# Kernel tuning notes

Measured on AMD Instinct MI355X. Metric: run time of the kernel, lower is better.

Reference implementation:

```python
import jax, jax.numpy as jnp
import numpy as np

EMBED = 768
N_HEADS = 12
HEAD = EMBED // N_HEADS  # 64
B, T = 2, 2048


def setup_inputs() -> dict:
    key = jax.random.key(0)
    ks = jax.random.split(key, 5)
    s = 0.02
    return {
        "x": jax.random.normal(ks[0], (B, T, EMBED), dtype=jnp.float32),
        "w_attn": jax.random.normal(ks[1], (EMBED, 3 * EMBED), dtype=jnp.float32) * s,
        "b_attn": jnp.zeros((3 * EMBED,), dtype=jnp.float32),
        "w_proj": jax.random.normal(ks[2], (EMBED, EMBED), dtype=jnp.float32) * s,
        "b_proj": jnp.zeros((EMBED,), dtype=jnp.float32),
    }


def reference(x, w_attn, b_attn, w_proj, b_proj):
    b, t, c = x.shape
    scale = HEAD ** -0.5
    qkv = x @ w_attn + b_attn  # [b,t,3c]
    q, k, v = jnp.split(qkv, 3, axis=-1)

    # einops 'b t (h n) -> b n t h' with n=N_HEADS: channel dim factors as
    # (head_size, n_heads) — head index is the inner factor.
    def split_heads(u):
        return u.reshape(b, t, HEAD, N_HEADS).transpose(0, 3, 1, 2)  # [b,n,t,h]

    q, k, v = split_heads(q), split_heads(k), split_heads(v)

    scores = jnp.einsum("bnth,bnsh->bnts", q, k) * scale  # [b,n,t,t]
    causal = jnp.tril(jnp.ones((t, t), dtype=bool))
    scores = jnp.where(causal, scores, jnp.finfo(scores.dtype).min)
    weights = jax.nn.softmax(scores, axis=-1)
    att = jnp.einsum("bnts,bnsh->bnth", weights, v)  # [b,n,t,h]

    # 'b n t h -> b t (n h)': heads are the OUTER factor on output
    att = att.transpose(0, 2, 1, 3).reshape(b, t, c)
    return att @ w_proj + b_proj
```

## Files before the change

kernel.cpp:

```cpp
#include <hip/hip_runtime.h>
#include <hip/hip_bf16.h>
#include <math.h>

#define NB      2
#define T_SZ    2048
#define EMBEDC  768
#define NHEADS  12
#define HEADD   64
#define QKV_PER (NB * NHEADS * T_SZ * HEADD)
#define QSCALE  0.18033688011112042f

typedef __bf16 bf16x8 __attribute__((ext_vector_type(8)));
typedef float  f32x4  __attribute__((ext_vector_type(4)));
typedef float  f32x16 __attribute__((ext_vector_type(16)));

__device__ inline ushort f2bf(float x) {
    union { float f; uint u; } v; v.f = x;
    uint r = v.u + 0x7fffu + ((v.u >> 16) & 1u);
    return (ushort)(r >> 16);
}

__device__ inline uint pack2bf(float a, float b) {
    union { __bf16 h[2]; uint u; } t;
    t.h[0] = (__bf16)a; t.h[1] = (__bf16)b;
    return t.u;
}

__device__ inline float bflo(uint u) {
    union { uint u; float f; } t; t.u = u << 16; return t.f;
}
__device__ inline float bfhi(uint u) {
    union { uint u; float f; } t; t.u = u & 0xffff0000u; return t.f;
}

__device__ inline void gload16(const ushort* g, ushort* l) {
    __builtin_amdgcn_global_load_lds(
        (const __attribute__((address_space(1))) unsigned int*)g,
        (__attribute__((address_space(3))) unsigned int*)l, 16, 0, 0);
}

__global__ __launch_bounds__(256) void cast_k(const float* __restrict__ in,
                                              ushort* __restrict__ out, int n)
{
    int i = (blockIdx.x * 256 + threadIdx.x) * 8;
    if (i >= n) return;
    float4 a = *(const float4*)(in + i);
    float4 b = *(const float4*)(in + i + 4);
    union { ushort u[8]; int4 v; } p;
    p.u[0] = f2bf(a.x); p.u[1] = f2bf(a.y); p.u[2] = f2bf(a.z); p.u[3] = f2bf(a.w);
    p.u[4] = f2bf(b.x); p.u[5] = f2bf(b.y); p.u[6] = f2bf(b.z); p.u[7] = f2bf(b.w);
    *(int4*)(out + i) = p.v;
}

template <int PERM>
__global__ __launch_bounds__(256) void tcast_k(const float* __restrict__ in,
                                               ushort* __restrict__ out,
                                               int R, int C)
{
    __shared__ float t[32][33];
    const int c0 = blockIdx.x * 32, r0 = blockIdx.y * 32;
    const int tx = threadIdx.x & 31, ty = threadIdx.x >> 5;
#pragma unroll
    for (int u = 0; u < 4; ++u)
        t[ty + 8 * u][tx] = in[(size_t)(r0 + ty + 8 * u) * C + c0 + tx];
    __syncthreads();
#pragma unroll
    for (int u = 0; u < 4; ++u) {
        int n = c0 + ty + 8 * u;
        int orow = n;
        if (PERM) {
            int mat = n / EMBEDC, cc = n % EMBEDC;
            orow = mat * EMBEDC + (cc % NHEADS) * HEADD + cc / NHEADS;
        }
        out[(size_t)orow * R + r0 + tx] = f2bf(t[tx][ty + 8 * u]);
    }
}

__global__ __launch_bounds__(256) void vt_k(const ushort* __restrict__ in,
                                            ushort* __restrict__ out)
{
    __shared__ ushort tile[64][66];
    const int bh = blockIdx.y;
    const int t0 = blockIdx.x * 64;
    const int tid = threadIdx.x;
#pragma unroll
    for (int u = 0; u < 2; ++u) {
        int s = tid + 256 * u;
        int r = s >> 3, c8 = s & 7;
        *(bf16x8*)&tile[r][c8 * 8] =
            *(const bf16x8*)(in + ((size_t)bh * T_SZ + t0 + r) * HEADD + c8 * 8);
    }
    __syncthreads();
#pragma unroll
    for (int u = 0; u < 2; ++u) {
        int s = tid + 256 * u;
        int hd = s >> 3, tt = s & 7;
        union { ushort v[8]; int4 q; } pk;
#pragma unroll
        for (int j = 0; j < 8; ++j) pk.v[j] = tile[tt * 8 + j][hd];
        *(int4*)(out + ((size_t)bh * HEADD + hd) * T_SZ + t0 + tt * 8) = pk.q;
    }
}

#define STAGE(buf, koff)                                        \
    do {                                                        \
        gload16(gA0 + (koff), &As[buf][lA0o]);                  \
        gload16(gA1 + (koff), &As[buf][lA1o]);                  \
        gload16(gB0 + (koff), &Bs[buf][lB0o]);                  \
        gload16(gB1 + (koff), &Bs[buf][lB1o]);                  \
    } while (0)

template <int MODE>
__global__ __launch_bounds__(256) void gemm_bf16_k(
    const ushort* __restrict__ A, const ushort* __restrict__ Bt,
    const float* __restrict__ bias, void* __restrict__ outp,
    int M, int N, int K)
{
    __shared__ ushort As[2][128 * 32];
    __shared__ ushort Bs[2][128 * 32];

    const int tid = threadIdx.x;
    const int w = tid >> 6, l = tid & 63;
    const int g = l >> 4, r16 = l & 15;
    const int wr = w >> 1, wc = w & 1;
    const int m0 = blockIdx.y * 128, n0 = blockIdx.x * 128;

    const int srow = l >> 2;
    const int scol = ((l & 3) ^ (srow & 3)) * 8;
    const ushort* gA0 = A + (size_t)(m0 + 32 * w + srow) * K + scol;
    const ushort* gA1 = gA0 + (size_t)16 * K;
    const ushort* gB0 = Bt + (size_t)(n0 + 32 * w + srow) * K + scol;
    const ushort* gB1 = gB0 + (size_t)16 * K;
    const int lA0o = (32 * w) * 32,      lA1o = (32 * w + 16) * 32;
    const int lB0o = lA0o,               lB1o = lA1o;

    f32x4 acc[4][4];
#pragma unroll
    for (int i = 0; i < 4; ++i)
#pragma unroll
        for (int j = 0; j < 4; ++j) acc[i][j] = (f32x4){0.f, 0.f, 0.f, 0.f};

    const int rck = (r16 & 3);

    STAGE(0, 0);
    __syncthreads();

    int cur = 0;
    for (int k0 = 0; k0 < K; k0 += 32) {
        if (k0 + 32 < K) STAGE(cur ^ 1, k0 + 32);

        const ushort* sA = As[cur];
        const ushort* sB = Bs[cur];
        bf16x8 af[4], bfr[4];
#pragma unroll
        for (int ms = 0; ms < 4; ++ms) {
            int row = 64 * wr + 16 * ms + r16;
            af[ms] = *(const bf16x8*)&sA[row * 32 + ((g ^ rck) * 8)];
        }
#pragma unroll
        for (int ns = 0; ns < 4; ++ns) {
            int row = 64 * wc + 16 * ns + r16;
            bfr[ns] = *(const bf16x8*)&sB[row * 32 + ((g ^ rck) * 8)];
        }
#pragma unroll
        for (int ms = 0; ms < 4; ++ms)
#pragma unroll
            for (int ns = 0; ns < 4; ++ns)
                acc[ms][ns] = __builtin_amdgcn_mfma_f32_16x16x32_bf16(
                    af[ms], bfr[ns], acc[ms][ns], 0, 0, 0);

        __syncthreads();
        cur ^= 1;
    }

#pragma unroll
    for (int ns = 0; ns < 4; ++ns) {
        const int n = n0 + 64 * wc + 16 * ns + r16;
        if (MODE == 0) {
            float* out = (float*)outp;
            const float bv = bias[n];
#pragma unroll
            for (int ms = 0; ms < 4; ++ms) {
                const int mb = m0 + 64 * wr + 16 * ms + 4 * g;
#pragma unroll
                for (int r = 0; r < 4; ++r)
                    out[(size_t)(mb + r) * N + n] = acc[ms][ns][r] + bv;
            }
        } else {
            ushort* ob = (ushort*)outp;
            const int mat  = n / EMBEDC;
            const int c    = n - mat * EMBEDC;
            const int head = c >> 6;
            const int hd   = c & 63;
            const float bv = bias[mat * EMBEDC + hd * NHEADS + head];
            const float qs = (mat == 0) ? QSCALE : 1.f;
#pragma unroll
            for (int ms = 0; ms < 4; ++ms) {
                const int mb = m0 + 64 * wr + 16 * ms + 4 * g;
#pragma unroll
                for (int r = 0; r < 4; ++r) {
                    const int m = mb + r;
                    const int b = m >> 11, t = m & 2047;
                    const size_t bh = (size_t)(b * NHEADS + head);
                    ob[(size_t)mat * QKV_PER + (bh * T_SZ + t) * HEADD + hd] =
                        f2bf((acc[ms][ns][r] + bv) * qs);
                }
            }
        }
    }
}

__global__ __launch_bounds__(512) void attn_mfma_k(
    const ushort* __restrict__ Qb, const ushort* __restrict__ Kb,
    const ushort* __restrict__ Vtb, ushort* __restrict__ Out)
{
    __shared__ ushort imgs[8 * 32 * 64];
    __shared__ float Ll[8 * 32];

    const int bid = blockIdx.x;
    const int xcd = bid & 7, j = bid >> 3;
    const int bh = xcd * 3 + (j >> 6);
    const int iq = 63 - (j & 63);
    const int bb = bh / NHEADS, head = bh % NHEADS;
    const int tid = threadIdx.x;
    const int w = tid >> 6, l = tid & 63;
    const int q31 = l & 31, hi = l >> 5;
    const int q0 = iq * 32;
    const int nt = iq + 1;
    const int cpw = (nt + 7) >> 3;
    const int b0 = w * cpw;
    const int b1 = min(b0 + cpw, nt);

    const ushort* Qg = Qb + (size_t)bh * T_SZ * HEADD;
    const ushort* Kg = Kb + (size_t)bh * T_SZ * HEADD;
    const ushort* Vg = Vtb + (size_t)bh * HEADD * T_SZ;
    const ushort* V0 = Vg + (size_t)q31 * T_SZ + 8 * hi;
    const ushort* V1 = Vg + (size_t)(32 + q31) * T_SZ + 8 * hi;

    f32x16 o0, o1, z;
#pragma unroll
    for (int r = 0; r < 16; ++r) { o0[r] = 0.f; o1[r] = 0.f; z[r] = 0.f; }
    float lR = 0.f;

    if (b0 < b1) {
        const ushort* qrow = Qg + (size_t)(q0 + q31) * HEADD + 8 * hi;
        const bf16x8 qf0 = *(const bf16x8*)(qrow);
        const bf16x8 qf1 = *(const bf16x8*)(qrow + 16);
        const bf16x8 qf2 = *(const bf16x8*)(qrow + 32);
        const bf16x8 qf3 = *(const bf16x8*)(qrow + 48);

        const ushort* Krow = Kg + (size_t)q31 * HEADD + 8 * hi;
        const ushort* kr0 = Krow + (size_t)(b0 * 32) * HEADD;
        bf16x8 kf0 = *(const bf16x8*)(kr0);
        bf16x8 kf1 = *(const bf16x8*)(kr0 + 16);
        bf16x8 kf2 = *(const bf16x8*)(kr0 + 32);
        bf16x8 kf3 = *(const bf16x8*)(kr0 + 48);

        for (int kt = b0; kt < b1; ++kt) {
            const int kvb = kt * 32;
            const bf16x8 va0 = *(const bf16x8*)(V0 + kvb);
            const bf16x8 va1 = *(const bf16x8*)(V0 + kvb + 16);
            const bf16x8 vb0 = *(const bf16x8*)(V1 + kvb);
            const bf16x8 vb1 = *(const bf16x8*)(V1 + kvb + 16);
            bf16x8 kn0, kn1, kn2, kn3;
            if (kt + 1 < b1) {
                const ushort* kr = Krow + (size_t)(kvb + 32) * HEADD;
                kn0 = *(const bf16x8*)(kr);
                kn1 = *(const bf16x8*)(kr + 16);
                kn2 = *(const bf16x8*)(kr + 32);
                kn3 = *(const bf16x8*)(kr + 48);
            }

            f32x16 st = z;
            st = __builtin_amdgcn_mfma_f32_32x32x16_bf16(kf0, qf0, st, 0, 0, 0);
            st = __builtin_amdgcn_mfma_f32_32x32x16_bf16(kf1, qf1, st, 0, 0, 0);
            st = __builtin_amdgcn_mfma_f32_32x32x16_bf16(kf2, qf2, st, 0, 0, 0);
            st = __builtin_amdgcn_mfma_f32_32x32x16_bf16(kf3, qf3, st, 0, 0, 0);

            if (kt == nt - 1) {
#pragma unroll
                for (int r = 0; r < 16; ++r)
                    if (((r & 3) + 8 * (r >> 2) + 4 * hi) > q31)
                        st[r] = -1e30f;
            }

            float rs = 0.f;
#pragma unroll
            for (int r = 0; r < 16; ++r) {
                float e = exp2f(st[r]);
                st[r] = e;
                rs += e;
            }
            rs += __shfl_xor(rs, 32);
            lR += rs;

            uint w0 = pack2bf(st[0],  st[1]),  w1 = pack2bf(st[2],  st[3]);
            uint w2 = pack2bf(st[4],  st[5]),  w3 = pack2bf(st[6],  st[7]);
            uint w4 = pack2bf(st[8],  st[9]),  w5 = pack2bf(st[10], st[11]);
            uint w6 = pack2bf(st[12], st[13]), w7 = pack2bf(st[14], st[15]);

            uint e0 = (uint)__shfl_xor((int)(hi ? w0 : w2), 32);
            uint e1 = (uint)__shfl_xor((int)(hi ? w1 : w3), 32);
            uint e2 = (uint)__shfl_xor((int)(hi ? w4 : w6), 32);
            uint e3 = (uint)__shfl_xor((int)(hi ? w5 : w7), 32);

            union { uint u[4]; bf16x8 v; } p0, p1;
            p0.u[0] = hi ? e0 : w0;  p0.u[1] = hi ? e1 : w1;
            p0.u[2] = hi ? w2 : e0;  p0.u[3] = hi ? w3 : e1;
            p1.u[0] = hi ? e2 : w4;  p1.u[1] = hi ? e3 : w5;
            p1.u[2] = hi ? w6 : e2;  p1.u[3] = hi ? w7 : e3;

            o0 = __builtin_amdgcn_mfma_f32_32x32x16_bf16(va0, p0.v, o0, 0, 0, 0);
            o0 = __builtin_amdgcn_mfma_f32_32x32x16_bf16(va1, p1.v, o0, 0, 0, 0);
            o1 = __builtin_amdgcn_mfma_f32_32x32x16_bf16(vb0, p0.v, o1, 0, 0, 0);
            o1 = __builtin_amdgcn_mfma_f32_32x32x16_bf16(vb1, p1.v, o1, 0, 0, 0);

            kf0 = kn0; kf1 = kn1; kf2 = kn2; kf3 = kn3;
        }
    }

    if (hi == 0) Ll[w * 32 + q31] = lR;
    const int key = 4 * (q31 & 15);
    ushort* img = &imgs[(w * 32 + q31) * 64];
#pragma unroll
    for (int c = 0; c < 4; ++c) {
        uint2 s0, s1;
        s0.x = pack2bf(o0[4 * c + 0], o0[4 * c + 1]);
        s0.y = pack2bf(o0[4 * c + 2], o0[4 * c + 3]);
        s1.x = pack2bf(o1[4 * c + 0], o1[4 * c + 1]);
        s1.y = pack2bf(o1[4 * c + 2], o1[4 * c + 3]);
        *(uint2*)&img[(8 * c + 4 * hi) ^ key]        = s0;
        *(uint2*)&img[((8 * c + 4 * hi) + 32) ^ key] = s1;
    }
    __syncthreads();

    {
        const int q  = tid >> 4;
        const int dg = tid & 15;
        const int gkey = 4 * (q & 15);
        const int dsw = (dg * 4) ^ gkey;
        float a0 = 0.f, a1 = 0.f, a2 = 0.f, a3 = 0.f, lt = 0.f;
#pragma unroll
        for (int ww = 0; ww < 8; ++ww) {
            lt += Ll[ww * 32 + q];
            uint2 pv = *(const uint2*)&imgs[(ww * 32 + q) * 64 + dsw];
            a0 += bflo(pv.x); a1 += bfhi(pv.x);
            a2 += bflo(pv.y); a3 += bfhi(pv.y);
        }
        const float inv = 1.f / lt;
        uint2 o;
        o.x = pack2bf(a0 * inv, a1 * inv);
        o.y = pack2bf(a2 * inv, a3 * inv);
        *(uint2*)(Out + ((size_t)(bb * T_SZ + q0 + q)) * EMBEDC
                  + head * HEADD + dg * 4) = o;
    }
}

extern "C" void kernel_launch(void* const* d_in, const int* in_sizes, int n_in,
                              void* d_out, int out_size, void* d_ws, size_t ws_size,
                              hipStream_t stream)
{
    const float* x      = (const float*)d_in[0];
    const float* w_attn = (const float*)d_in[1];
    const float* b_attn = (const float*)d_in[2];
    const float* w_proj = (const float*)d_in[3];
    const float* b_proj = (const float*)d_in[4];
    float* out = (float*)d_out;

    ushort* qw   = (ushort*)d_ws;
    ushort* vT   = qw + (size_t)3 * QKV_PER;
    ushort* attb = vT + QKV_PER;
    ushort* xb   = attb + QKV_PER;
    ushort* waT  = xb + QKV_PER;
    ushort* wpT  = waT + (size_t)EMBEDC * 3 * EMBEDC;

    cast_k<<<QKV_PER / (256 * 8), 256, 0, stream>>>(x, xb, QKV_PER);
    tcast_k<1><<<dim3(3 * EMBEDC / 32, EMBEDC / 32), 256, 0, stream>>>(
        w_attn, waT, EMBEDC, 3 * EMBEDC);
    tcast_k<0><<<dim3(EMBEDC / 32, EMBEDC / 32), 256, 0, stream>>>(
        w_proj, wpT, EMBEDC, EMBEDC);

    gemm_bf16_k<1><<<dim3(2304 / 128, 4096 / 128), 256, 0, stream>>>(
        xb, waT, b_attn, qw, NB * T_SZ, 3 * EMBEDC, EMBEDC);

    vt_k<<<dim3(T_SZ / 64, NB * NHEADS), 256, 0, stream>>>(
        qw + 2 * (size_t)QKV_PER, vT);

    attn_mfma_k<<<1536, 512, 0, stream>>>(
        qw, qw + QKV_PER, vT, attb);

    gemm_bf16_k<0><<<dim3(768 / 128, 4096 / 128), 256, 0, stream>>>(
        attb, wpT, b_proj, out, NB * T_SZ, EMBEDC, EMBEDC);
}
```

Before: 128.3 us.

## Pair light and heavy causal query tiles per block and drop P-operand shuffles

Each attention block now handles two query tiles, p and 63-p, so every block does about the same amount of causal work, and the grid is halved to 768 blocks. The V^T operand is loaded as split 8-byte pieces in an order that matches the MFMA accumulator layout of P. This removes the per-iteration cross-half shuffles and selects used to rearrange the probabilities. The row-sum shuffle moves out of the inner loop. In exchange there is an extra block-wide sync between the two tiles, half as many blocks for latency hiding, and narrower V loads.

```diff
diff --git a/kernel.cpp b/kernel.cpp
--- a/kernel.cpp
+++ b/kernel.cpp
@@ -219,140 +219,145 @@
 
     const int bid = blockIdx.x;
     const int xcd = bid & 7, j = bid >> 3;
-    const int bh = xcd * 3 + (j >> 6);
-    const int iq = 63 - (j & 63);
+    const int bh = xcd * 3 + (j >> 5);
+    const int p  = j & 31;
     const int bb = bh / NHEADS, head = bh % NHEADS;
     const int tid = threadIdx.x;
     const int w = tid >> 6, l = tid & 63;
     const int q31 = l & 31, hi = l >> 5;
-    const int q0 = iq * 32;
-    const int nt = iq + 1;
-    const int cpw = (nt + 7) >> 3;
-    const int b0 = w * cpw;
-    const int b1 = min(b0 + cpw, nt);
 
     const ushort* Qg = Qb + (size_t)bh * T_SZ * HEADD;
     const ushort* Kg = Kb + (size_t)bh * T_SZ * HEADD;
     const ushort* Vg = Vtb + (size_t)bh * HEADD * T_SZ;
-    const ushort* V0 = Vg + (size_t)q31 * T_SZ + 8 * hi;
-    const ushort* V1 = Vg + (size_t)(32 + q31) * T_SZ + 8 * hi;
-
-    f32x16 o0, o1, z;
-#pragma unroll
-    for (int r = 0; r < 16; ++r) { o0[r] = 0.f; o1[r] = 0.f; z[r] = 0.f; }
-    float lR = 0.f;
-
-    if (b0 < b1) {
-        const ushort* qrow = Qg + (size_t)(q0 + q31) * HEADD + 8 * hi;
-        const bf16x8 qf0 = *(const bf16x8*)(qrow);
-        const bf16x8 qf1 = *(const bf16x8*)(qrow + 16);
-        const bf16x8 qf2 = *(const bf16x8*)(qrow + 32);
-        const bf16x8 qf3 = *(const bf16x8*)(qrow + 48);
-
-        const ushort* Krow = Kg + (size_t)q31 * HEADD + 8 * hi;
-        const ushort* kr0 = Krow + (size_t)(b0 * 32) * HEADD;
-        bf16x8 kf0 = *(const bf16x8*)(kr0);
-        bf16x8 kf1 = *(const bf16x8*)(kr0 + 16);
-        bf16x8 kf2 = *(const bf16x8*)(kr0 + 32);
-        bf16x8 kf3 = *(const bf16x8*)(kr0 + 48);
-
-        for (int kt = b0; kt < b1; ++kt) {
-            const int kvb = kt * 32;
-            const bf16x8 va0 = *(const bf16x8*)(V0 + kvb);
-            const bf16x8 va1 = *(const bf16x8*)(V0 + kvb + 16);
-            const bf16x8 vb0 = *(const bf16x8*)(V1 + kvb);
-            const bf16x8 vb1 = *(const bf16x8*)(V1 + kvb + 16);
-            bf16x8 kn0, kn1, kn2, kn3;
-            if (kt + 1 < b1) {
-                const ushort* kr = Krow + (size_t)(kvb + 32) * HEADD;
-                kn0 = *(const bf16x8*)(kr);
-                kn1 = *(const bf16x8*)(kr + 16);
-                kn2 = *(const bf16x8*)(kr + 32);
-                kn3 = *(const bf16x8*)(kr + 48);
+    const ushort* Va = Vg + (size_t)q31 * T_SZ + 4 * hi;
+    const ushort* Vb = Vg + (size_t)(32 + q31) * T_SZ + 4 * hi;
+    const ushort* Krow = Kg + (size_t)q31 * HEADD + 8 * hi;
+
+    for (int rep = 0; rep < 2; ++rep) {
+        const int iq = rep ? (63 - p) : p;
+        const int q0 = iq * 32;
+        const int nt = iq + 1;
+        const int cpw = (nt + 7) >> 3;
+        const int b0 = w * cpw;
+        const int b1 = min(b0 + cpw, nt);
+
+        f32x16 o0, o1, z;
+#pragma unroll
+        for (int r = 0; r < 16; ++r) { o0[r] = 0.f; o1[r] = 0.f; z[r] = 0.f; }
+        float lR = 0.f;
+
+        if (b0 < b1) {
+            const ushort* qrow = Qg + (size_t)(q0 + q31) * HEADD + 8 * hi;
+            const bf16x8 qf0 = *(const bf16x8*)(qrow);
+            const bf16x8 qf1 = *(const bf16x8*)(qrow + 16);
+            const bf16x8 qf2 = *(const bf16x8*)(qrow + 32);
+            const bf16x8 qf3 = *(const bf16x8*)(qrow + 48);
+
+            const ushort* kr0 = Krow + (size_t)(b0 * 32) * HEADD;
+            bf16x8 kf0 = *(const bf16x8*)(kr0);
+            bf16x8 kf1 = *(const bf16x8*)(kr0 + 16);
+            bf16x8 kf2 = *(const bf16x8*)(kr0 + 32);
+            bf16x8 kf3 = *(const bf16x8*)(kr0 + 48);
+
+            for (int kt = b0; kt < b1; ++kt) {
+                const int kvb = kt * 32;
+                union U8 { uint2 d[2]; bf16x8 v; };
+                U8 va0, va1, vb0, vb1;
+                va0.d[0] = *(const uint2*)(Va + kvb);
+                va0.d[1] = *(const uint2*)(Va + kvb + 8);
+                va1.d[0] = *(const uint2*)(Va + kvb + 16);
+                va1.d[1] = *(const uint2*)(Va + kvb + 24);
+                vb0.d[0] = *(const uint2*)(Vb + kvb);
+                vb0.d[1] = *(const uint2*)(Vb + kvb + 8);
+                vb1.d[0] = *(const uint2*)(Vb + kvb + 16);
+                vb1.d[1] = *(const uint2*)(Vb + kvb + 24);
+                bf16x8 kn0, kn1, kn2, kn3;
+                if (kt + 1 < b1) {
+                    const ushort* kr = Krow + (size_t)(kvb + 32) * HEADD;
+                    kn0 = *(const bf16x8*)(kr);
+                    kn1 = *(const bf16x8*)(kr + 16);
+                    kn2 = *(const bf16x8*)(kr + 32);
+                    kn3 = *(const bf16x8*)(kr + 48);
+                }
+
+                f32x16 st = z;
+                st = __builtin_amdgcn_mfma_f32_32x32x16_bf16(kf0, qf0, st, 0, 0, 0);
+                st = __builtin_amdgcn_mfma_f32_32x32x16_bf16(kf1, qf1, st, 0, 0, 0);
+                st = __builtin_amdgcn_mfma_f32_32x32x16_bf16(kf2, qf2, st, 0, 0, 0);
+                st = __builtin_amdgcn_mfma_f32_32x32x16_bf16(kf3, qf3, st, 0, 0, 0);
+
+                if (kt == nt - 1) {
+#pragma unroll
+                    for (int r = 0; r < 16; ++r)
+                        if (((r & 3) + 8 * (r >> 2) + 4 * hi) > q31)
+                            st[r] = -1e30f;
+                }
+
+                float rs = 0.f;
+#pragma unroll
+                for (int r = 0; r < 16; ++r) {
+                    float e = exp2f(st[r]);
+                    st[r] = e;
+                    rs += e;
+                }
+                lR += rs;
+
+                union { uint u[4]; bf16x8 v; } B1, B2;
+                B1.u[0] = pack2bf(st[0],  st[1]);
+                B1.u[1] = pack2bf(st[2],  st[3]);
+                B1.u[2] = pack2bf(st[4],  st[5]);
+                B1.u[3] = pack2bf(st[6],  st[7]);
+                B2.u[0] = pack2bf(st[8],  st[9]);
+                B2.u[1] = pack2bf(st[10], st[11]);
+                B2.u[2] = pack2bf(st[12], st[13]);
+                B2.u[3] = pack2bf(st[14], st[15]);
+
+                o0 = __builtin_amdgcn_mfma_f32_32x32x16_bf16(va0.v, B1.v, o0, 0, 0, 0);
+                o0 = __builtin_amdgcn_mfma_f32_32x32x16_bf16(va1.v, B2.v, o0, 0, 0, 0);
+                o1 = __builtin_amdgcn_mfma_f32_32x32x16_bf16(vb0.v, B1.v, o1, 0, 0, 0);
+                o1 = __builtin_amdgcn_mfma_f32_32x32x16_bf16(vb1.v, B2.v, o1, 0, 0, 0);
+
+                kf0 = kn0; kf1 = kn1; kf2 = kn2; kf3 = kn3;
             }
-
-            f32x16 st = z;
-            st = __builtin_amdgcn_mfma_f32_32x32x16_bf16(kf0, qf0, st, 0, 0, 0);
-            st = __builtin_amdgcn_mfma_f32_32x32x16_bf16(kf1, qf1, st, 0, 0, 0);
-            st = __builtin_amdgcn_mfma_f32_32x32x16_bf16(kf2, qf2, st, 0, 0, 0);
-            st = __builtin_amdgcn_mfma_f32_32x32x16_bf16(kf3, qf3, st, 0, 0, 0);
-
-            if (kt == nt - 1) {
-#pragma unroll
-                for (int r = 0; r < 16; ++r)
-                    if (((r & 3) + 8 * (r >> 2) + 4 * hi) > q31)
-                        st[r] = -1e30f;
+            lR += __shfl_xor(lR, 32);
+        }
+
+        if (rep) __syncthreads();
+        if (hi == 0) Ll[w * 32 + q31] = lR;
+        const int key = 4 * (q31 & 15);
+        ushort* img = &imgs[(w * 32 + q31) * 64];
+#pragma unroll
+        for (int c = 0; c < 4; ++c) {
+            uint2 s0, s1;
+            s0.x = pack2bf(o0[4 * c + 0], o0[4 * c + 1]);
+            s0.y = pack2bf(o0[4 * c + 2], o0[4 * c + 3]);
+            s1.x = pack2bf(o1[4 * c + 0], o1[4 * c + 1]);
+            s1.y = pack2bf(o1[4 * c + 2], o1[4 * c + 3]);
+            *(uint2*)&img[(8 * c + 4 * hi) ^ key]        = s0;
+            *(uint2*)&img[((8 * c + 4 * hi) + 32) ^ key] = s1;
+        }
+        __syncthreads();
+
+        {
+            const int q  = tid >> 4;
+            const int dg = tid & 15;
+            const int gkey = 4 * (q & 15);
+            const int dsw = (dg * 4) ^ gkey;
+            float a0 = 0.f, a1 = 0.f, a2 = 0.f, a3 = 0.f, lt = 0.f;
+#pragma unroll
+            for (int ww = 0; ww < 8; ++ww) {
+                lt += Ll[ww * 32 + q];
+                uint2 pv = *(const uint2*)&imgs[(ww * 32 + q) * 64 + dsw];
+                a0 += bflo(pv.x); a1 += bfhi(pv.x);
+                a2 += bflo(pv.y); a3 += bfhi(pv.y);
             }
-
-            float rs = 0.f;
-#pragma unroll
-            for (int r = 0; r < 16; ++r) {
-                float e = exp2f(st[r]);
-                st[r] = e;
-                rs += e;
-            }
-            rs += __shfl_xor(rs, 32);
-            lR += rs;
-
-            uint w0 = pack2bf(st[0],  st[1]),  w1 = pack2bf(st[2],  st[3]);
-            uint w2 = pack2bf(st[4],  st[5]),  w3 = pack2bf(st[6],  st[7]);
-            uint w4 = pack2bf(st[8],  st[9]),  w5 = pack2bf(st[10], st[11]);
-            uint w6 = pack2bf(st[12], st[13]), w7 = pack2bf(st[14], st[15]);
-
-            uint e0 = (uint)__shfl_xor((int)(hi ? w0 : w2), 32);
-            uint e1 = (uint)__shfl_xor((int)(hi ? w1 : w3), 32);
-            uint e2 = (uint)__shfl_xor((int)(hi ? w4 : w6), 32);
-            uint e3 = (uint)__shfl_xor((int)(hi ? w5 : w7), 32);
-
-            union { uint u[4]; bf16x8 v; } p0, p1;
-            p0.u[0] = hi ? e0 : w0;  p0.u[1] = hi ? e1 : w1;
-            p0.u[2] = hi ? w2 : e0;  p0.u[3] = hi ? w3 : e1;
-            p1.u[0] = hi ? e2 : w4;  p1.u[1] = hi ? e3 : w5;
-            p1.u[2] = hi ? w6 : e2;  p1.u[3] = hi ? w7 : e3;
-
-            o0 = __builtin_amdgcn_mfma_f32_32x32x16_bf16(va0, p0.v, o0, 0, 0, 0);
-            o0 = __builtin_amdgcn_mfma_f32_32x32x16_bf16(va1, p1.v, o0, 0, 0, 0);
-            o1 = __builtin_amdgcn_mfma_f32_32x32x16_bf16(vb0, p0.v, o1, 0, 0, 0);
-            o1 = __builtin_amdgcn_mfma_f32_32x32x16_bf16(vb1, p1.v, o1, 0, 0, 0);
-
-            kf0 = kn0; kf1 = kn1; kf2 = kn2; kf3 = kn3;
-        }
-    }
-
-    if (hi == 0) Ll[w * 32 + q31] = lR;
-    const int key = 4 * (q31 & 15);
-    ushort* img = &imgs[(w * 32 + q31) * 64];
-#pragma unroll
-    for (int c = 0; c < 4; ++c) {
-        uint2 s0, s1;
-        s0.x = pack2bf(o0[4 * c + 0], o0[4 * c + 1]);
-        s0.y = pack2bf(o0[4 * c + 2], o0[4 * c + 3]);
-        s1.x = pack2bf(o1[4 * c + 0], o1[4 * c + 1]);
-        s1.y = pack2bf(o1[4 * c + 2], o1[4 * c + 3]);
-        *(uint2*)&img[(8 * c + 4 * hi) ^ key]        = s0;
-        *(uint2*)&img[((8 * c + 4 * hi) + 32) ^ key] = s1;
-    }
-    __syncthreads();
-
-    {
-        const int q  = tid >> 4;
-        const int dg = tid & 15;
-        const int gkey = 4 * (q & 15);
-        const int dsw = (dg * 4) ^ gkey;
-        float a0 = 0.f, a1 = 0.f, a2 = 0.f, a3 = 0.f, lt = 0.f;
-#pragma unroll
-        for (int ww = 0; ww < 8; ++ww) {
-            lt += Ll[ww * 32 + q];
-            uint2 pv = *(const uint2*)&imgs[(ww * 32 + q) * 64 + dsw];
-            a0 += bflo(pv.x); a1 += bfhi(pv.x);
-            a2 += bflo(pv.y); a3 += bfhi(pv.y);
-        }
-        const float inv = 1.f / lt;
-        uint2 o;
-        o.x = pack2bf(a0 * inv, a1 * inv);
-        o.y = pack2bf(a2 * inv, a3 * inv);
-        *(uint2*)(Out + ((size_t)(bb * T_SZ + q0 + q)) * EMBEDC
-                  + head * HEADD + dg * 4) = o;
+            const float inv = 1.f / lt;
+            uint2 o;
+            o.x = pack2bf(a0 * inv, a1 * inv);
+            o.y = pack2bf(a2 * inv, a3 * inv);
+            *(uint2*)(Out + ((size_t)(bb * T_SZ + q0 + q)) * EMBEDC
+                      + head * HEADD + dg * 4) = o;
+        }
     }
 }
 
@@ -386,7 +391,7 @@
     vt_k<<<dim3(T_SZ / 64, NB * NHEADS), 256, 0, stream>>>(
         qw + 2 * (size_t)QKV_PER, vT);
 
-    attn_mfma_k<<<1536, 512, 0, stream>>>(
+    attn_mfma_k<<<768, 512, 0, stream>>>(
         qw, qw + QKV_PER, vT, attb);
 
     gemm_bf16_k<0><<<dim3(768 / 128, 4096 / 128), 256, 0, stream>>>(
```

Result: slower. 145.0 us (+13.0%).
